# Performance work log

Measured on AMD Instinct MI355X. Metric: run time of the kernel, lower is better.

The kernel has to match this reference:

```python
import jax, jax.numpy as jnp
import numpy as np

EMB, GRU_H, HID = 256, 256, 256


def _gru_dir(x_sbe, h0, W_ih, W_hh, b_ih, b_hh):
    # x_sbe: (S,B,E); W_ih: (3H,E); W_hh: (3H,H); biases: (3H,)
    # PyTorch gate order: r, z, n
    gx = jnp.einsum('sbe,ge->sbg', x_sbe, W_ih) + b_ih  # (S,B,3H) precomputed input gates
    H = W_hh.shape[1]

    def step(h, gx_t):
        gh = h @ W_hh.T + b_hh
        xr, xz, xn = gx_t[..., :H], gx_t[..., H:2 * H], gx_t[..., 2 * H:]
        hr, hz, hn = gh[..., :H], gh[..., H:2 * H], gh[..., 2 * H:]
        r = jax.nn.sigmoid(xr + hr)
        z = jax.nn.sigmoid(xz + hz)
        n = jnp.tanh(xn + r * hn)
        h_new = (1.0 - z) * n + z * h
        return h_new, h_new

    hT, ys = jax.lax.scan(step, h0, gx)
    return ys, hT  # ys: (S,B,H), hT: (B,H)


def setup_inputs() -> dict:
    key = jax.random.key(0)
    ks = jax.random.split(key, 12)
    B, S = 64, 1024
    s = 1.0 / np.sqrt(GRU_H)
    u = lambda k, shp: jax.random.uniform(k, shp, jnp.float32, -s, s)
    return {
        'X': jax.random.normal(ks[0], (B, S, EMB), jnp.float32),
        'W_ih_f': u(ks[1], (3 * GRU_H, EMB)),
        'W_hh_f': u(ks[2], (3 * GRU_H, GRU_H)),
        'b_ih_f': u(ks[3], (3 * GRU_H,)),
        'b_hh_f': u(ks[4], (3 * GRU_H,)),
        'W_ih_b': u(ks[5], (3 * GRU_H, EMB)),
        'W_hh_b': u(ks[6], (3 * GRU_H, GRU_H)),
        'b_ih_b': u(ks[7], (3 * GRU_H,)),
        'b_hh_b': u(ks[8], (3 * GRU_H,)),
        'W_fc': u(ks[9], (HID, 2 * GRU_H)),
        'b_fc': u(ks[10], (HID,)),
    }


def reference(X, W_ih_f, W_hh_f, b_ih_f, b_hh_f, W_ih_b, W_hh_b, b_ih_b, b_hh_b, W_fc, b_fc):
    x = jnp.transpose(X, (1, 0, 2))  # (S,B,E)
    S, B, _ = x.shape
    h0 = jnp.zeros((B, GRU_H), x.dtype)
    out_f, hT_f = _gru_dir(x, h0, W_ih_f, W_hh_f, b_ih_f, b_hh_f)
    out_b_rev, hT_b = _gru_dir(x[::-1], h0, W_ih_b, W_hh_b, b_ih_b, b_hh_b)
    out_b = out_b_rev[::-1]
    outputs = jnp.concatenate([out_f, out_b], axis=-1)  # (S,B,2H)
    hidden_state = jnp.stack([hT_f, hT_b], axis=0)      # (2,B,H)
    outputs = jax.nn.relu(jnp.einsum('sbk,hk->sbh', outputs, W_fc) + b_fc)
    return outputs, hidden_state
```

## Files before the change

kernel.cpp:

```cpp
#include <hip/hip_runtime.h>
#include <hip/hip_fp16.h>


typedef _Float16 f16x8 __attribute__((ext_vector_type(8)));
typedef _Float16 f16x4 __attribute__((ext_vector_type(4)));
typedef float    f32x4 __attribute__((ext_vector_type(4)));

#define MFMA(a,b,c) __builtin_amdgcn_mfma_f32_16x16x32_f16((a),(b),(c),0,0,0)
#define SWZ(r,c)  ((((r)*512)  + (c)) ^ (((r)&7)<<4))
#define SWZ2(r,c) ((((r)*1024) + (c)) ^ (((r)&7)<<4))

#define NLOG2E (-1.442695041f)
#define P2LOG2E (2.885390082f)

__device__ inline f16x8 pack8(float4 a, float4 b){
  f16x8 h;
  h[0]=(_Float16)a.x; h[1]=(_Float16)a.y; h[2]=(_Float16)a.z; h[3]=(_Float16)a.w;
  h[4]=(_Float16)b.x; h[5]=(_Float16)b.y; h[6]=(_Float16)b.z; h[7]=(_Float16)b.w;
  return h;
}
__device__ inline f16x8 pack8s(float4 a, float4 b, float s){
  f16x8 h;
  h[0]=(_Float16)(a.x*s); h[1]=(_Float16)(a.y*s); h[2]=(_Float16)(a.z*s); h[3]=(_Float16)(a.w*s);
  h[4]=(_Float16)(b.x*s); h[5]=(_Float16)(b.y*s); h[6]=(_Float16)(b.z*s); h[7]=(_Float16)(b.w*s);
  return h;
}

__device__ __forceinline__ void gx_body(
    char* smem, const float* __restrict__ X,
    const float* __restrict__ Wp, const float* __restrict__ bi, const float* __restrict__ bh,
    _Float16* __restrict__ gxc, int CT, int tc, int dir, int t)
{
  _Float16* As = (_Float16*)smem;
  _Float16* Bs = (_Float16*)(smem + 32768);
  const int tid = threadIdx.x;
  #pragma unroll
  for (int i = 0; i < 4; ++i) {
    int c = tid + i*512, r = c >> 5, cc = c & 31;
    const float4* s4 = (const float4*)(X + ((size_t)r*1024 + t)*256 + cc*8);
    *(f16x8*)((char*)As + SWZ(r, cc*16)) = pack8(s4[0], s4[1]);
  }
  const int w = tid >> 6, l = tid & 63, lr = l & 15, g = l >> 4;
  const size_t obase = (((size_t)dir*CT + tc)*4 + (w & 3)) * (size_t)12288;
  #pragma unroll 1
  for (int nt = 0; nt < 12; ++nt) {
    __syncthreads();
    #pragma unroll
    for (int i = 0; i < 4; ++i) {
      int c = tid + i*512, r = c >> 5, cc = c & 31;
      const float4* s4 = (const float4*)(Wp + (size_t)(nt*64 + r)*256 + cc*8);
      *(f16x8*)((char*)Bs + SWZ(r, cc*16)) = pack8(s4[0], s4[1]);
    }
    __syncthreads();
    if (w < 4) {
      f32x4 acc[4];
      #pragma unroll
      for (int ct = 0; ct < 4; ++ct) acc[ct] = (f32x4){0.f,0.f,0.f,0.f};
      #pragma unroll
      for (int kk = 0; kk < 8; ++kk) {
        f16x8 af = *(const f16x8*)((const char*)As + SWZ(w*16 + lr, kk*64 + g*16));
        #pragma unroll
        for (int ct = 0; ct < 4; ++ct) {
          f16x8 bfr = *(const f16x8*)((const char*)Bs + SWZ(ct*16 + lr, kk*64 + g*16));
          acc[ct] = MFMA(af, bfr, acc[ct]);
        }
      }
      #pragma unroll
      for (int ct = 0; ct < 4; ++ct) {
        const int col = nt*64 + ct*16 + lr;
        const int gate = col >> 8;
        const float sc = (gate == 2) ? P2LOG2E : NLOG2E;
        const float bv = bi[col] + (gate < 2 ? bh[col] : 0.f);
        const int j = col & 255;
        const int tid2 = (j>>5)*64 + g*16 + (j&15);
        const int off = ((j>>4)&1)*4;
        f16x4 v;
        #pragma unroll
        for (int q = 0; q < 4; ++q) v[q] = (_Float16)((acc[ct][q] + bv)*sc);
        *(f16x4*)(gxc + obase + (size_t)tid2*24 + gate*8 + off) = v;
      }
    }
  }
}

__global__ __launch_bounds__(512, 2) void k_gx0(
    const float* __restrict__ X,
    const float* __restrict__ Wf, const float* __restrict__ bihf, const float* __restrict__ bhhf,
    const float* __restrict__ Wb, const float* __restrict__ bihb, const float* __restrict__ bhhb,
    _Float16* __restrict__ gxc, int CT, int sbase)
{
  __shared__ char smem[65536];
  const int tc = blockIdx.x, dir = blockIdx.y;
  const int p = sbase + tc;
  const int t = dir ? (1023 - p) : p;
  gx_body(smem, X, dir ? Wb : Wf, dir ? bihb : bihf, dir ? bhhb : bhhf,
          gxc, CT, tc, dir, t);
}

__global__ __launch_bounds__(512, 2) void k_step(
    const float* __restrict__ Whh_f, const float* __restrict__ bhh_f,
    const float* __restrict__ Whh_b, const float* __restrict__ bhh_b,
    const _Float16* __restrict__ gxin, float* __restrict__ wsh,
    _Float16* __restrict__ out16, float* __restrict__ hidden,
    int CT, int sbase,
    const float* __restrict__ X,
    const float* __restrict__ Wf, const float* __restrict__ bihf, const float* __restrict__ bhhf,
    const float* __restrict__ Wb, const float* __restrict__ bihb, const float* __restrict__ bhhb,
    _Float16* __restrict__ gxout, int sbase_gx, int gx_valid)
{
  __shared__ char smem[65536];
  if (blockIdx.x >= 8) {
    if (!gx_valid) return;
    const int b = blockIdx.x - 8;
    const int tc = b >> 1, dir = b & 1;
    const int p = sbase_gx + tc;
    const int t = dir ? (1023 - p) : p;
    gx_body(smem, X, dir ? Wb : Wf, dir ? bihb : bihf, dir ? bhhb : bhhf,
            gxout, CT, tc, dir, t);
    return;
  }
  const int dir = blockIdx.x & 1;
  const int bsl = blockIdx.x >> 1;
  const int bbase = bsl * 16;
  const float* __restrict__ Whh = dir ? Whh_b : Whh_f;
  const float* __restrict__ bhh = dir ? bhh_b : bhh_f;
  const int tid = threadIdx.x, w = tid >> 6, l = tid & 63;
  const int lr = l & 15, g = l >> 4;
  const int j0 = w * 32;
  f16x8 wf[6][8];
  #pragma unroll
  for (int ct = 0; ct < 6; ++ct) {
    const int colg = (ct>>1)*256 + j0 + (ct&1)*16 + lr;
    const float scl = (ct < 4) ? NLOG2E : P2LOG2E;
    #pragma unroll
    for (int kk = 0; kk < 8; ++kk) {
      const float4* s4 = (const float4*)(Whh + (size_t)colg*256 + kk*32 + g*8);
      wf[ct][kk] = pack8s(s4[0], s4[1], scl);
    }
  }
  const float bn0 = P2LOG2E * bhh[512 + j0 + lr];
  const float bn1 = P2LOG2E * bhh[512 + j0 + 16 + lr];
  char* const hsb = smem;
  char* const afp = hsb + l*16;
  char* const hwp = hsb + w*1024 + (lr>>3)*256 + g*64 + (lr&7)*2;
  float hold[2][4];
  if (sbase == 0) {
    *(int4*)(hsb + tid*16) = make_int4(0,0,0,0);
    #pragma unroll
    for (int jt = 0; jt < 2; ++jt)
      #pragma unroll
      for (int q = 0; q < 4; ++q) hold[jt][q] = 0.f;
  } else {
    const int r = tid >> 5, kq = tid & 31;
    const float4* s4 = (const float4*)(wsh + ((size_t)(dir*64 + bbase + r))*256 + kq*8);
    *(f16x8*)(hsb + (kq>>2)*1024 + (((kq&3)*16) + r)*16) = pack8(s4[0], s4[1]);
    #pragma unroll
    for (int jt = 0; jt < 2; ++jt)
      #pragma unroll
      for (int q = 0; q < 4; ++q)
        hold[jt][q] = wsh[((size_t)(dir*64 + bbase + g*4 + q))*256 + j0 + jt*16 + lr];
  }
  __syncthreads();
  if (w & 1) __builtin_amdgcn_s_setprio(1);

  const int t0 = dir ? (1023 - sbase) : sbase;
  char* optr = (char*)out16 + ((size_t)t0*64 + bbase + g*4)*1024
             + (size_t)(dir*256 + j0 + lr)*2;
  const ptrdiff_t ostep = dir ? -(ptrdiff_t)65536 : (ptrdiff_t)65536;
  const _Float16* gp = gxin + ((size_t)(dir*CT)*4 + bsl)*12288 + (size_t)tid*24;
  const ptrdiff_t gstep = 4*12288;

#define REC_STEP(RB)                                                               \
  {                                                                                \
    const f16x8 gv0 = *(const f16x8*)(gp);                                         \
    const f16x8 gv1 = *(const f16x8*)(gp + 8);                                     \
    const f16x8 gv2 = *(const f16x8*)(gp + 16);                                    \
    gp += gstep;                                                                   \
    {                                                                              \
      f32x4 ar = (f32x4){0.f,0.f,0.f,0.f};                                         \
      f32x4 az = (f32x4){0.f,0.f,0.f,0.f};                                         \
      f32x4 an = (f32x4){bn0,bn0,bn0,bn0};                                         \
      _Pragma("unroll")                                                            \
      for (int kk = 0; kk < 8; ++kk) {                                             \
        const f16x8 af = *(const f16x8*)(afp + (RB)*8192 + kk*1024);               \
        ar = MFMA(af, wf[0][kk], ar);                                              \
        az = MFMA(af, wf[2][kk], az);                                              \
        an = MFMA(af, wf[4][kk], an);                                              \
      }                                                                            \
      _Pragma("unroll")                                                            \
      for (int q = 0; q < 4; ++q) {                                                \
        const float rv = __builtin_amdgcn_rcpf(                                    \
            1.f + __builtin_amdgcn_exp2f((float)gv0[q] + ar[q]));                  \
        const float zv = __builtin_amdgcn_rcpf(                                    \
            1.f + __builtin_amdgcn_exp2f((float)gv1[q] + az[q]));                  \
        const float nv = __builtin_fmaf(-2.f, __builtin_amdgcn_rcpf(               \
            1.f + __builtin_amdgcn_exp2f(                                          \
                __builtin_fmaf(rv, an[q], (float)gv2[q]))), 1.f);                  \
        const float h = __builtin_fmaf(zv, hold[0][q] - nv, nv);                   \
        hold[0][q] = h;                                                            \
        const _Float16 hf = (_Float16)h;                                           \
        *(_Float16*)(hwp + ((RB)^1)*8192 + q*16) = hf;                             \
        *(_Float16*)(optr + q*1024) = hf;                                          \
      }                                                                            \
    }                                                                              \
    {                                                                              \
      f32x4 ar = (f32x4){0.f,0.f,0.f,0.f};                                         \
      f32x4 az = (f32x4){0.f,0.f,0.f,0.f};                                         \
      f32x4 an = (f32x4){bn1,bn1,bn1,bn1};                                         \
      _Pragma("unroll")                                                            \
      for (int kk = 0; kk < 8; ++kk) {                                             \
        const f16x8 af = *(const f16x8*)(afp + (RB)*8192 + kk*1024);               \
        ar = MFMA(af, wf[1][kk], ar);                                              \
        az = MFMA(af, wf[3][kk], az);                                              \
        an = MFMA(af, wf[5][kk], an);                                              \
      }                                                                            \
      _Pragma("unroll")                                                            \
      for (int q = 0; q < 4; ++q) {                                                \
        const float rv = __builtin_amdgcn_rcpf(                                    \
            1.f + __builtin_amdgcn_exp2f((float)gv0[4+q] + ar[q]));                \
        const float zv = __builtin_amdgcn_rcpf(                                    \
            1.f + __builtin_amdgcn_exp2f((float)gv1[4+q] + az[q]));                \
        const float nv = __builtin_fmaf(-2.f, __builtin_amdgcn_rcpf(               \
            1.f + __builtin_amdgcn_exp2f(                                          \
                __builtin_fmaf(rv, an[q], (float)gv2[4+q]))), 1.f);                \
        const float h = __builtin_fmaf(zv, hold[1][q] - nv, nv);                   \
        hold[1][q] = h;                                                            \
        const _Float16 hf = (_Float16)h;                                           \
        *(_Float16*)(hwp + ((RB)^1)*8192 + 512 + q*16) = hf;                       \
        *(_Float16*)(optr + q*1024 + 32) = hf;                                     \
      }                                                                            \
    }                                                                              \
    optr += ostep;                                                                 \
    asm volatile("s_waitcnt lgkmcnt(0)" ::: "memory");                             \
    __builtin_amdgcn_s_barrier();                                                  \
    asm volatile("" ::: "memory");                                                 \
  }

  #pragma unroll 1
  for (int sc = 0; sc < CT; sc += 2) {
    REC_STEP(0)
    REC_STEP(1)
  }
#undef REC_STEP

  if (sbase + CT == 1024) {
    #pragma unroll
    for (int jt = 0; jt < 2; ++jt)
      #pragma unroll
      for (int q = 0; q < 4; ++q)
        hidden[((size_t)(dir*64 + bbase + g*4 + q))*256 + j0 + jt*16 + lr] = hold[jt][q];
  } else {
    #pragma unroll
    for (int jt = 0; jt < 2; ++jt)
      #pragma unroll
      for (int q = 0; q < 4; ++q)
        wsh[((size_t)(dir*64 + bbase + g*4 + q))*256 + j0 + jt*16 + lr] = hold[jt][q];
  }
}

__global__ __launch_bounds__(256) void k_fc(
    const _Float16* __restrict__ h16, const float* __restrict__ Wfc,
    const float* __restrict__ bfc, float* __restrict__ out)
{
  const int mt = blockIdx.x;
  __shared__ _Float16 As[64*512];
  const int tid = threadIdx.x, w = tid >> 6, l = tid & 63;
  const int lr = l & 15, g = l >> 4;
  #pragma unroll
  for (int i = 0; i < 16; ++i) {
    int c = tid + i*256, r = c >> 6, cc = c & 63;
    *(int4*)((char*)As + SWZ2(r, cc*16)) =
        *(const int4*)((const char*)h16 + ((size_t)mt*64 + r)*1024 + cc*16);
  }
  __syncthreads();
  #pragma unroll 1
  for (int nt = 0; nt < 4; ++nt) {
    f32x4 acc[4];
    #pragma unroll
    for (int ct = 0; ct < 4; ++ct) acc[ct] = (f32x4){0.f,0.f,0.f,0.f};
    #pragma unroll 2
    for (int kk = 0; kk < 16; ++kk) {
      f16x8 af = *(const f16x8*)((const char*)As + SWZ2(w*16 + lr, kk*64 + g*16));
      #pragma unroll
      for (int ct = 0; ct < 4; ++ct) {
        const float4* s4 = (const float4*)(Wfc + (size_t)(nt*64 + ct*16 + lr)*512 + kk*32 + g*8);
        acc[ct] = MFMA(af, pack8(s4[0], s4[1]), acc[ct]);
      }
    }
    #pragma unroll
    for (int ct = 0; ct < 4; ++ct) {
      const int col = nt*64 + ct*16 + lr;
      const float bv = bfc[col];
      #pragma unroll
      for (int q = 0; q < 4; ++q) {
        const int row = w*16 + g*4 + q;
        out[((size_t)mt*64 + row)*256 + col] = fmaxf(acc[ct][q] + bv, 0.f);
      }
    }
  }
}

extern "C" void kernel_launch(void* const* d_in, const int* in_sizes, int n_in,
                              void* d_out, int out_size, void* d_ws, size_t ws_size,
                              hipStream_t stream) {
  const float* X      = (const float*)d_in[0];
  const float* W_ih_f = (const float*)d_in[1];
  const float* W_hh_f = (const float*)d_in[2];
  const float* b_ih_f = (const float*)d_in[3];
  const float* b_hh_f = (const float*)d_in[4];
  const float* W_ih_b = (const float*)d_in[5];
  const float* W_hh_b = (const float*)d_in[6];
  const float* b_ih_b = (const float*)d_in[7];
  const float* b_hh_b = (const float*)d_in[8];
  const float* W_fc   = (const float*)d_in[9];
  const float* b_fc   = (const float*)d_in[10];

  int CT = 256;
  while (CT > 8 && (2*(size_t)CT*196608 + 131072) > ws_size) CT >>= 1;
  const size_t CTB = (size_t)CT*196608;
  _Float16* buf0 = (_Float16*)d_ws;
  _Float16* buf1 = (_Float16*)((char*)d_ws + CTB);
  float*    wsh  = (float*)((char*)d_ws + 2*CTB);

  _Float16* h16   = (_Float16*)d_out;
  float*    out   = (float*)d_out;
  float*    hidden= (float*)d_out + (size_t)1024*64*256;

  const int NC = 1024 / CT;
  k_gx0<<<dim3(CT, 2), dim3(512), 0, stream>>>(X, W_ih_f, b_ih_f, b_hh_f,
                                               W_ih_b, b_ih_b, b_hh_b, buf0, CT, 0);
  for (int c = 0; c < NC; ++c) {
    _Float16* bin  = (c & 1) ? buf1 : buf0;
    _Float16* bout = (c & 1) ? buf0 : buf1;
    k_step<<<dim3(8 + 2*CT), dim3(512), 0, stream>>>(
        W_hh_f, b_hh_f, W_hh_b, b_hh_b, bin, wsh, h16, hidden, CT, c*CT,
        X, W_ih_f, b_ih_f, b_hh_f, W_ih_b, b_ih_b, b_hh_b,
        bout, (c+1)*CT, (c < NC-1) ? 1 : 0);
  }
  k_fc<<<dim3(1024), dim3(256), 0, stream>>>(h16, W_fc, b_fc, out);
}
```

Measured before the change: 2.105 ms.

## Overlap FC projection with recurrent steps for timesteps whose both directions are finished

The final FC+ReLU projection is split into tiles by timestep. Tiles whose forward and backward hidden states are already complete are issued as extra blocks inside the last recurrent step launches. The remaining tiles run in a tail kernel that uses 512-thread blocks. This hides part of the FC work behind the latency-bound recurrence, which occupies only a few blocks. It also removes the wave priority boost in the recurrent loop, which risks slowing the critical serial path while FC blocks compete for the same hardware.

```diff
diff --git a/kernel.cpp b/kernel.cpp
--- a/kernel.cpp
+++ b/kernel.cpp
@@ -9,7 +9,6 @@
 #define MFMA(a,b,c) __builtin_amdgcn_mfma_f32_16x16x32_f16((a),(b),(c),0,0,0)
 #define SWZ(r,c)  ((((r)*512)  + (c)) ^ (((r)&7)<<4))
 #define SWZ2(r,c) ((((r)*1024) + (c)) ^ (((r)&7)<<4))
-
 #define NLOG2E (-1.442695041f)
 #define P2LOG2E (2.885390082f)
 
@@ -83,6 +82,50 @@
   }
 }
 
+__device__ __forceinline__ void fc_body(
+    char* smem, const _Float16* __restrict__ h16, const float* __restrict__ Wfc,
+    const float* __restrict__ bfc, float* __restrict__ out, int mt)
+{
+  _Float16* As = (_Float16*)smem;
+  const int tid = threadIdx.x, w = tid >> 6, l = tid & 63;
+  const int lr = l & 15, g = l >> 4;
+  #pragma unroll
+  for (int i = 0; i < 8; ++i) {
+    int c = tid + i*512, r = c >> 6, cc = c & 63;
+    *(int4*)((char*)As + SWZ2(r, cc*16)) =
+        *(const int4*)((const char*)h16 + ((size_t)mt*64 + r)*1024 + cc*16);
+  }
+  __syncthreads();
+  const int w4 = w & 3;
+  const int nb = (w >> 2) * 2;
+  #pragma unroll 1
+  for (int ni = 0; ni < 2; ++ni) {
+    const int nt = nb + ni;
+    f32x4 acc[4];
+    #pragma unroll
+    for (int ct = 0; ct < 4; ++ct) acc[ct] = (f32x4){0.f,0.f,0.f,0.f};
+    #pragma unroll 2
+    for (int kk = 0; kk < 16; ++kk) {
+      f16x8 af = *(const f16x8*)((const char*)As + SWZ2(w4*16 + lr, kk*64 + g*16));
+      #pragma unroll
+      for (int ct = 0; ct < 4; ++ct) {
+        const float4* s4 = (const float4*)(Wfc + (size_t)(nt*64 + ct*16 + lr)*512 + kk*32 + g*8);
+        acc[ct] = MFMA(af, pack8(s4[0], s4[1]), acc[ct]);
+      }
+    }
+    #pragma unroll
+    for (int ct = 0; ct < 4; ++ct) {
+      const int col = nt*64 + ct*16 + lr;
+      const float bv = bfc[col];
+      #pragma unroll
+      for (int q = 0; q < 4; ++q) {
+        const int row = w4*16 + g*4 + q;
+        out[((size_t)mt*64 + row)*256 + col] = fmaxf(acc[ct][q] + bv, 0.f);
+      }
+    }
+  }
+}
+
 __global__ __launch_bounds__(512, 2) void k_gx0(
     const float* __restrict__ X,
     const float* __restrict__ Wf, const float* __restrict__ bihf, const float* __restrict__ bhhf,
@@ -106,9 +149,17 @@
     const float* __restrict__ X,
     const float* __restrict__ Wf, const float* __restrict__ bihf, const float* __restrict__ bhhf,
     const float* __restrict__ Wb, const float* __restrict__ bihb, const float* __restrict__ bhhb,
-    _Float16* __restrict__ gxout, int sbase_gx, int gx_valid)
+    _Float16* __restrict__ gxout, int sbase_gx, int gx_valid,
+    const float* __restrict__ Wfc, const float* __restrict__ bfc,
+    float* __restrict__ outf, int fb1, int fn1, int fb2)
 {
   __shared__ char smem[65536];
+  if (blockIdx.x >= (unsigned)(8 + 2*CT)) {
+    const int i = blockIdx.x - (8 + 2*CT);
+    const int mt = (i < fn1) ? (fb1 + i) : (fb2 + (i - fn1));
+    fc_body(smem, out16, Wfc, bfc, outf, mt);
+    return;
+  }
   if (blockIdx.x >= 8) {
     if (!gx_valid) return;
     const int b = blockIdx.x - 8;
@@ -161,7 +212,6 @@
         hold[jt][q] = wsh[((size_t)(dir*64 + bbase + g*4 + q))*256 + j0 + jt*16 + lr];
   }
   __syncthreads();
-  if (w & 1) __builtin_amdgcn_s_setprio(1);
 
   const int t0 = dir ? (1023 - sbase) : sbase;
   char* optr = (char*)out16 + ((size_t)t0*64 + bbase + g*4)*1024
@@ -258,46 +308,15 @@
   }
 }
 
-__global__ __launch_bounds__(256) void k_fc(
+__global__ __launch_bounds__(512, 2) void k_fc_tail(
     const _Float16* __restrict__ h16, const float* __restrict__ Wfc,
-    const float* __restrict__ bfc, float* __restrict__ out)
-{
-  const int mt = blockIdx.x;
-  __shared__ _Float16 As[64*512];
-  const int tid = threadIdx.x, w = tid >> 6, l = tid & 63;
-  const int lr = l & 15, g = l >> 4;
-  #pragma unroll
-  for (int i = 0; i < 16; ++i) {
-    int c = tid + i*256, r = c >> 6, cc = c & 63;
-    *(int4*)((char*)As + SWZ2(r, cc*16)) =
-        *(const int4*)((const char*)h16 + ((size_t)mt*64 + r)*1024 + cc*16);
-  }
-  __syncthreads();
-  #pragma unroll 1
-  for (int nt = 0; nt < 4; ++nt) {
-    f32x4 acc[4];
-    #pragma unroll
-    for (int ct = 0; ct < 4; ++ct) acc[ct] = (f32x4){0.f,0.f,0.f,0.f};
-    #pragma unroll 2
-    for (int kk = 0; kk < 16; ++kk) {
-      f16x8 af = *(const f16x8*)((const char*)As + SWZ2(w*16 + lr, kk*64 + g*16));
-      #pragma unroll
-      for (int ct = 0; ct < 4; ++ct) {
-        const float4* s4 = (const float4*)(Wfc + (size_t)(nt*64 + ct*16 + lr)*512 + kk*32 + g*8);
-        acc[ct] = MFMA(af, pack8(s4[0], s4[1]), acc[ct]);
-      }
-    }
-    #pragma unroll
-    for (int ct = 0; ct < 4; ++ct) {
-      const int col = nt*64 + ct*16 + lr;
-      const float bv = bfc[col];
-      #pragma unroll
-      for (int q = 0; q < 4; ++q) {
-        const int row = w*16 + g*4 + q;
-        out[((size_t)mt*64 + row)*256 + col] = fmaxf(acc[ct][q] + bv, 0.f);
-      }
-    }
-  }
+    const float* __restrict__ bfc, float* __restrict__ out,
+    int fb1, int fn1, int fb2)
+{
+  __shared__ char smem[65536];
+  const int i = blockIdx.x;
+  const int mt = (i < fn1) ? (fb1 + i) : (fb2 + (i - fn1));
+  fc_body(smem, h16, Wfc, bfc, out, mt);
 }
 
 extern "C" void kernel_launch(void* const* d_in, const int* in_sizes, int n_in,
@@ -329,13 +348,26 @@
   const int NC = 1024 / CT;
   k_gx0<<<dim3(CT, 2), dim3(512), 0, stream>>>(X, W_ih_f, b_ih_f, b_hh_f,
                                                W_ih_b, b_ih_b, b_hh_b, buf0, CT, 0);
+  int flo = 512, fhi = 512;
   for (int c = 0; c < NC; ++c) {
     _Float16* bin  = (c & 1) ? buf1 : buf0;
     _Float16* bout = (c & 1) ? buf0 : buf1;
-    k_step<<<dim3(8 + 2*CT), dim3(512), 0, stream>>>(
+    const int alo = 1024 - c*CT, ahi = c*CT;
+    int b1 = 0, n1 = 0, b2 = 0, n2 = 0;
+    if (ahi > alo) {
+      if (alo < flo) { b1 = alo; n1 = flo - alo; }
+      if (ahi > fhi) { b2 = fhi; n2 = ahi - fhi; }
+      if (alo < flo) flo = alo;
+      if (ahi > fhi) fhi = ahi;
+    }
+    k_step<<<dim3(8 + 2*CT + n1 + n2), dim3(512), 0, stream>>>(
         W_hh_f, b_hh_f, W_hh_b, b_hh_b, bin, wsh, h16, hidden, CT, c*CT,
         X, W_ih_f, b_ih_f, b_hh_f, W_ih_b, b_ih_b, b_hh_b,
-        bout, (c+1)*CT, (c < NC-1) ? 1 : 0);
-  }
-  k_fc<<<dim3(1024), dim3(256), 0, stream>>>(h16, W_fc, b_fc, out);
-}
+        bout, (c+1)*CT, (c < NC-1) ? 1 : 0,
+        W_fc, b_fc, out, b1, n1, b2);
+  }
+  const int tn1 = flo, tn2 = 1024 - fhi;
+  if (tn1 + tn2 > 0)
+    k_fc_tail<<<dim3(tn1 + tn2), dim3(512), 0, stream>>>(h16, W_fc, b_fc, out,
+                                                         0, tn1, fhi);
+}
```

Result: no change. 2.088 ms (-0.8%).
